# Optimization experiments

Measured on AMD Instinct MI355X. Metric: run time of the kernel, lower is better.

## Reference

```python
import jax, jax.numpy as jnp
import numpy as np

N_NODES = 100000
N_EDGES = 1600000
N_GRAPHS = 64


def setup_inputs() -> dict:
    key = jax.random.key(0)
    ks = jax.random.split(key, 10)
    x = jax.random.normal(ks[0], (N_NODES, 2), jnp.float32)
    edge_index = jax.random.randint(ks[1], (2, N_EDGES), 0, N_NODES, dtype=jnp.int64)
    batch_index = jnp.sort(jax.random.randint(ks[2], (N_NODES,), 0, N_GRAPHS, dtype=jnp.int64))

    def glorot(k, shape):
        return jax.random.normal(k, shape, jnp.float32) * jnp.sqrt(2.0 / (shape[0] + shape[1]))

    return {
        "x": x,
        "edge_index": edge_index,
        "batch_index": batch_index,
        "W1": glorot(ks[3], (2, 8)),   "b1": jnp.zeros((8,), jnp.float32),
        "W2": glorot(ks[4], (8, 32)),  "b2": jnp.zeros((32,), jnp.float32),
        "W3": glorot(ks[5], (32, 128)),"b3": jnp.zeros((128,), jnp.float32),
        "Wl": glorot(ks[6], (128, 3)), "bl": jnp.zeros((3,), jnp.float32),
    }


def _gcn_conv(x, W, b, src, dst, norm, n):
    # GCNConv: linear transform, then normalized scatter-add aggregation, then bias.
    h = x @ W                                     # [N, out]
    msg = h[src] * norm[:, None]                  # [E', out] gather + scale
    agg = jax.ops.segment_sum(msg, dst, num_segments=n)
    return agg + b


def reference(x, edge_index, batch_index, W1, b1, W2, b2, W3, b3, Wl, bl):
    n = x.shape[0]
    loop = jnp.arange(n, dtype=edge_index.dtype)
    src = jnp.concatenate([edge_index[0], loop])  # add self-loops (GCNConv default)
    dst = jnp.concatenate([edge_index[1], loop])
    # symmetric normalization D^{-1/2} (A+I) D^{-1/2}
    deg = jax.ops.segment_sum(jnp.ones_like(dst, dtype=x.dtype), dst, num_segments=n)
    dis = jnp.where(deg > 0, jax.lax.rsqrt(jnp.maximum(deg, 1.0)), 0.0)
    norm = dis[src] * dis[dst]

    h = jax.nn.relu(_gcn_conv(x, W1, b1, src, dst, norm, n))
    h = jax.nn.relu(_gcn_conv(h, W2, b2, src, dst, norm, n))  # dropout is identity in eval
    h = _gcn_conv(h, W3, b3, src, dst, norm, n)               # [N, 128]
    pooled = jax.ops.segment_max(h, batch_index, num_segments=N_GRAPHS)  # global_max_pool
    logits = pooled @ Wl + bl                                  # [G, 3]
    return jax.nn.log_softmax(logits, axis=1)
```

## Files before the change

### kernel.cpp

```cpp
#include <hip/hip_runtime.h>


#define BSHIFT 9
#define BSZ 512
#define P2_TILE 2048
#define P1_BLOCKS 128

__device__ __forceinline__ unsigned fenc(float x) {
  unsigned b = __float_as_uint(x);
  return (b & 0x80000000u) ? ~b : (b | 0x80000000u);
}
__device__ __forceinline__ float fdec(unsigned k) {
  return (k & 0x80000000u) ? __uint_as_float(k ^ 0x80000000u)
                           : __uint_as_float(~k);
}


__global__ __launch_bounds__(256) void p1_hist_kernel(const int* __restrict__ dst,
                                                      int* __restrict__ hist2d, int E) {
  __shared__ int h[256];
  h[threadIdx.x] = 0;
  __syncthreads();
  for (int e = blockIdx.x * blockDim.x + threadIdx.x; e < E; e += gridDim.x * blockDim.x)
    atomicAdd(&h[dst[e] >> BSHIFT], 1);
  __syncthreads();
  hist2d[blockIdx.x * 256 + threadIdx.x] = h[threadIdx.x];
}

__global__ __launch_bounds__(256) void p1_scan_kernel(const int* __restrict__ hist2d,
                                                      int* __restrict__ bucketBase,
                                                      int* __restrict__ bucketCursor,
                                                      unsigned* __restrict__ pooled,
                                                      int B, int E, int G) {
  __shared__ int s[256];
  int t = threadIdx.x;
  int v = 0;
  for (int b = 0; b < P1_BLOCKS; ++b) v += hist2d[b * 256 + t];
  if (t >= B) v = 0;
  s[t] = v;
  __syncthreads();
  for (int o = 1; o < 256; o <<= 1) {
    int u = (t >= o) ? s[t - o] : 0;
    __syncthreads();
    s[t] += u;
    __syncthreads();
  }
  int excl = s[t] - v;
  bucketBase[t] = excl;
  bucketCursor[t] = excl;
  if (t == 0) bucketBase[256] = E;
  for (int i = t; i < G * 128; i += 256) pooled[i] = 0u;
}

__global__ __launch_bounds__(256) void p2_partition_kernel(
    const int* __restrict__ src, const int* __restrict__ dst,
    int* __restrict__ bucketCursor, unsigned* __restrict__ part, int E) {
  __shared__ int hist[256];
  __shared__ int lbase[256];
  __shared__ int gbase[256];
  __shared__ int cur[256];
  __shared__ unsigned sbuf[P2_TILE];
  __shared__ unsigned abuf[P2_TILE];
  int t = threadIdx.x;
  int e0 = blockIdx.x * P2_TILE;
  int cnt = min(P2_TILE, E - e0);

  hist[t] = 0;
  __syncthreads();

  int myb[P2_TILE / 256];
  unsigned myp[P2_TILE / 256];
#pragma unroll
  for (int k = 0; k < P2_TILE / 256; ++k) {
    int i = t + k * 256;
    if (i < cnt) {
      int e = e0 + i;
      int d = dst[e];
      int b = d >> BSHIFT;
      myb[k] = b;
      myp[k] = ((unsigned)(d & (BSZ - 1)) << 17) | (unsigned)src[e];
      atomicAdd(&hist[b], 1);
    } else {
      myb[k] = -1;
      myp[k] = 0;
    }
  }
  __syncthreads();

  int v = hist[t];
  lbase[t] = v;
  __syncthreads();
  for (int o = 1; o < 256; o <<= 1) {
    int u = (t >= o) ? lbase[t - o] : 0;
    __syncthreads();
    lbase[t] += u;
    __syncthreads();
  }
  int excl = lbase[t] - v;
  __syncthreads();
  lbase[t] = excl;
  if (v > 0) gbase[t] = atomicAdd(&bucketCursor[t], v);
  cur[t] = 0;
  __syncthreads();

#pragma unroll
  for (int k = 0; k < P2_TILE / 256; ++k) {
    int b = myb[k];
    if (b >= 0) {
      int pos = atomicAdd(&cur[b], 1);
      int li = lbase[b] + pos;
      sbuf[li] = myp[k];
      abuf[li] = (unsigned)(gbase[b] + pos);
    }
  }
  __syncthreads();

#pragma unroll
  for (int k = 0; k < P2_TILE / 256; ++k) {
    int i = t + k * 256;
    if (i < cnt) part[abuf[i]] = sbuf[i];
  }
}

__global__ __launch_bounds__(512) void p3_build_kernel(
    const unsigned* __restrict__ part, const int* __restrict__ bucketBase,
    const float* __restrict__ x, float* __restrict__ xs,
    float* __restrict__ dis, int* __restrict__ rp, int* __restrict__ csr,
    int N, int B, int E) {
  __shared__ int hist[BSZ];
  __shared__ int scn[BSZ];
  int b = blockIdx.x, t = threadIdx.x;
  int base = bucketBase[b], end = bucketBase[b + 1];
  int cnt = end - base;

  hist[t] = 0;
  __syncthreads();
  for (int i = t; i < cnt; i += BSZ) atomicAdd(&hist[part[base + i] >> 17], 1);
  __syncthreads();

  int v = hist[t];
  scn[t] = v;
  __syncthreads();
  for (int o = 1; o < BSZ; o <<= 1) {
    int u = (t >= o) ? scn[t - o] : 0;
    __syncthreads();
    scn[t] += u;
    __syncthreads();
  }
  int excl = scn[t] - v;

  int n = (b << BSHIFT) + t;
  if (n < N) {
    float dn = rsqrtf((float)v + 1.0f);
    dis[n] = dn;
    rp[n] = base + excl;
    float2 xn = *reinterpret_cast<const float2*>(x + 2 * (size_t)n);
    float2 o;
    o.x = dn * xn.x;
    o.y = dn * xn.y;
    *reinterpret_cast<float2*>(xs + 2 * (size_t)n) = o;
  }
  if (b == B - 1 && t == 0) rp[N] = E;

  hist[t] = excl;
  __syncthreads();
  for (int i = t; i < cnt; i += BSZ) {
    unsigned p = part[base + i];
    int pos = atomicAdd(&hist[p >> 17], 1);
    csr[base + pos] = (int)(p & 0x1FFFFu);
  }
}


__global__ __launch_bounds__(256) void layer1_kernel(
    const int* __restrict__ rp, const int* __restrict__ csr, const float* __restrict__ dis,
    const float* __restrict__ xs, const float* __restrict__ W1, const float* __restrict__ b1,
    float* __restrict__ h1s, int N) {
  __shared__ float sW[16];
  __shared__ float sb[8];
  int t = threadIdx.x;
  if (t < 16) sW[t] = W1[t];
  if (t < 8) sb[t] = b1[t];
  __syncthreads();
  int n = blockIdx.x * blockDim.x + t;
  if (n >= N) return;
  float2 a = *reinterpret_cast<const float2*>(xs + 2 * (size_t)n);
  int j0 = rp[n], j1 = rp[n + 1];
#pragma unroll 4
  for (int j = j0; j < j1; ++j) {
    int s = csr[j];
    const float2 v = *reinterpret_cast<const float2*>(xs + 2 * (size_t)s);
    a.x += v.x;
    a.y += v.y;
  }
  float dn = dis[n];
  float ax = dn * a.x, ay = dn * a.y;
  float4 o0, o1;
  float* o = &o0.x;
#pragma unroll
  for (int f = 0; f < 8; ++f)
    o[f] = dn * fmaxf(ax * sW[f] + ay * sW[8 + f] + sb[f], 0.f);
  *reinterpret_cast<float4*>(h1s + (size_t)n * 8) = o0;
  *reinterpret_cast<float4*>(h1s + (size_t)n * 8 + 4) = o1;
}

__global__ __launch_bounds__(256) void layer2_kernel(
    const int* __restrict__ rp, const int* __restrict__ csr, const float* __restrict__ dis,
    const float* __restrict__ h1s, const float* __restrict__ W2, const float* __restrict__ b2,
    float* __restrict__ h2s, int N) {
  __shared__ float sW[256];
  __shared__ float sb[32];
  int t = threadIdx.x;
  sW[t] = W2[t];
  if (t < 32) sb[t] = b2[t];
  __syncthreads();
  int n = blockIdx.x * blockDim.x + t;
  if (n >= N) return;
  float4 a0 = *reinterpret_cast<const float4*>(h1s + (size_t)n * 8);
  float4 a1 = *reinterpret_cast<const float4*>(h1s + (size_t)n * 8 + 4);
  int j0 = rp[n], j1 = rp[n + 1];
#pragma unroll 2
  for (int j = j0; j < j1; ++j) {
    int s = csr[j];
    const float4 v0 = *reinterpret_cast<const float4*>(h1s + (size_t)s * 8);
    const float4 v1 = *reinterpret_cast<const float4*>(h1s + (size_t)s * 8 + 4);
    a0.x += v0.x; a0.y += v0.y; a0.z += v0.z; a0.w += v0.w;
    a1.x += v1.x; a1.y += v1.y; a1.z += v1.z; a1.w += v1.w;
  }
  float dn = dis[n];
  float a2r[8] = {dn * a0.x, dn * a0.y, dn * a0.z, dn * a0.w,
                  dn * a1.x, dn * a1.y, dn * a1.z, dn * a1.w};
#pragma unroll
  for (int fc = 0; fc < 8; ++fc) {
    float4 o;
    o.x = sb[fc * 4 + 0]; o.y = sb[fc * 4 + 1]; o.z = sb[fc * 4 + 2]; o.w = sb[fc * 4 + 3];
#pragma unroll
    for (int k = 0; k < 8; ++k) {
      const float4 w = *reinterpret_cast<const float4*>(&sW[k * 32 + fc * 4]);
      float a = a2r[k];
      o.x += a * w.x; o.y += a * w.y; o.z += a * w.z; o.w += a * w.w;
    }
    o.x = dn * fmaxf(o.x, 0.f);
    o.y = dn * fmaxf(o.y, 0.f);
    o.z = dn * fmaxf(o.z, 0.f);
    o.w = dn * fmaxf(o.w, 0.f);
    *reinterpret_cast<float4*>(h2s + (size_t)n * 32 + fc * 4) = o;
  }
}

__global__ __launch_bounds__(128) void layer3_pool_kernel(
    const int* __restrict__ rp, const int* __restrict__ csr, const float* __restrict__ dis,
    const float* __restrict__ h2s, const float* __restrict__ W3, const float* __restrict__ b3,
    const int* __restrict__ batch, unsigned* __restrict__ pooled, int N) {
  __shared__ float rows[16][32];
  int t = threadIdx.x;
  float Wreg[32];
#pragma unroll
  for (int k = 0; k < 32; ++k) Wreg[k] = W3[k * 128 + t];
  float bb = b3[t];

  int n0 = blockIdx.x * 16;
  int m = min(16, N - n0);

  {
    int r = t >> 3;
    int n = n0 + r;
    if (r < m) {
      int off = (t & 7) * 4;
      float4 acc = *reinterpret_cast<const float4*>(h2s + (size_t)n * 32 + off);
      int j0 = rp[n], j1 = rp[n + 1];
#pragma unroll 4
      for (int j = j0; j < j1; ++j) {
        int s = csr[j];
        const float4 v = *reinterpret_cast<const float4*>(h2s + (size_t)s * 32 + off);
        acc.x += v.x; acc.y += v.y; acc.z += v.z; acc.w += v.w;
      }
      float dn = dis[n];
      rows[r][off + 0] = dn * acc.x;
      rows[r][off + 1] = dn * acc.y;
      rows[r][off + 2] = dn * acc.z;
      rows[r][off + 3] = dn * acc.w;
    }
  }
  __syncthreads();

  int curg = batch[n0];
  float runmax = -INFINITY;
  for (int r = 0; r < m; ++r) {
    int g = batch[n0 + r];
    if (g != curg) {
      atomicMax(&pooled[(size_t)curg * 128 + t], fenc(runmax));
      runmax = -INFINITY;
      curg = g;
    }
    float acc = bb;
#pragma unroll
    for (int k = 0; k < 32; ++k) acc += rows[r][k] * Wreg[k];
    runmax = fmaxf(runmax, acc);
  }
  atomicMax(&pooled[(size_t)curg * 128 + t], fenc(runmax));
}

__global__ __launch_bounds__(128) void head_kernel(
    const unsigned* __restrict__ pooled, const float* __restrict__ Wl,
    const float* __restrict__ bl, float* __restrict__ out, int G) {
  int g = blockIdx.x;
  int t = threadIdx.x;
  float p = fdec(pooled[(size_t)g * 128 + t]);
  __shared__ float red[128];
  __shared__ float sj[3];
  for (int j = 0; j < 3; ++j) {
    red[t] = p * Wl[t * 3 + j];
    __syncthreads();
    for (int k = 64; k > 0; k >>= 1) {
      if (t < k) red[t] += red[t + k];
      __syncthreads();
    }
    if (t == 0) sj[j] = red[0];
    __syncthreads();
  }
  if (t == 0) {
    float l0 = sj[0] + bl[0], l1 = sj[1] + bl[1], l2 = sj[2] + bl[2];
    float m = fmaxf(l0, fmaxf(l1, l2));
    float lse = logf(expf(l0 - m) + expf(l1 - m) + expf(l2 - m));
    out[g * 3 + 0] = l0 - m - lse;
    out[g * 3 + 1] = l1 - m - lse;
    out[g * 3 + 2] = l2 - m - lse;
  }
}

extern "C" void kernel_launch(void* const* d_in, const int* in_sizes, int n_in,
                              void* d_out, int out_size, void* d_ws, size_t ws_size,
                              hipStream_t stream) {
  const float* x = (const float*)d_in[0];
  const int* ei = (const int*)d_in[1];
  const int* batch = (const int*)d_in[2];
  const float* W1 = (const float*)d_in[3];
  const float* b1 = (const float*)d_in[4];
  const float* W2 = (const float*)d_in[5];
  const float* b2 = (const float*)d_in[6];
  const float* W3 = (const float*)d_in[7];
  const float* b3 = (const float*)d_in[8];
  const float* Wl = (const float*)d_in[9];
  const float* bl = (const float*)d_in[10];
  float* out = (float*)d_out;

  const int N = in_sizes[0] / 2;
  const int E = in_sizes[1] / 2;
  const int G = out_size / 3;

  const int* src = ei;
  const int* dstp = ei + E;

  const int B = (N + BSZ - 1) / BSZ;

  size_t NP = ((size_t)N + 256) & ~(size_t)255;
  size_t EP = ((size_t)E + 255) & ~(size_t)255;

  float* dis = (float*)d_ws;
  int* rp = (int*)d_ws + NP;
  int* csr = rp + NP;
  unsigned* part = (unsigned*)(csr + EP);
  int* bucketBase = (int*)(part + EP);
  int* bucketCursor = bucketBase + 512;
  int* hist2d = bucketCursor + 512;
  float* arena = (float*)(hist2d + P1_BLOCKS * 256);

  float* xs = arena;
  float* h1s = arena + (size_t)2 * N;
  float* h2s = arena + (size_t)10 * N;
  unsigned* pooled = (unsigned*)(arena + (size_t)42 * N);

  const int BS = 256;
  auto cdiv = [](long long a, long long b) { return (int)((a + b - 1) / b); };

  p1_hist_kernel<<<P1_BLOCKS, 256, 0, stream>>>(dstp, hist2d, E);
  p1_scan_kernel<<<1, 256, 0, stream>>>(hist2d, bucketBase, bucketCursor, pooled, B, E, G);
  p2_partition_kernel<<<cdiv(E, P2_TILE), 256, 0, stream>>>(src, dstp, bucketCursor, part, E);
  p3_build_kernel<<<B, BSZ, 0, stream>>>(part, bucketBase, x, xs, dis, rp, csr, N, B, E);

  layer1_kernel<<<cdiv(N, BS), BS, 0, stream>>>(rp, csr, dis, xs, W1, b1, h1s, N);
  layer2_kernel<<<cdiv(N, BS), BS, 0, stream>>>(rp, csr, dis, h1s, W2, b2, h2s, N);
  layer3_pool_kernel<<<cdiv(N, 16), 128, 0, stream>>>(rp, csr, dis, h2s, W3, b3, batch, pooled, N);

  head_kernel<<<G, 128, 0, stream>>>(pooled, Wl, bl, out, G);
}
```

Measured before the change: 147.8 us.

## Balance layer-3 gather across block edges using packed local-row ids in CSR

After: 388.4 us. 2.63x slower.

```diff
diff --git a/kernel.cpp b/kernel.cpp
--- a/kernel.cpp
+++ b/kernel.cpp
@@ -5,6 +5,7 @@
 #define BSZ 512
 #define P2_TILE 2048
 #define P1_BLOCKS 128
+#define SRCMASK 0x1FFFF
 
 __device__ __forceinline__ unsigned fenc(float x) {
   unsigned b = __float_as_uint(x);
@@ -125,7 +126,7 @@
 __global__ __launch_bounds__(512) void p3_build_kernel(
     const unsigned* __restrict__ part, const int* __restrict__ bucketBase,
     const float* __restrict__ x, float* __restrict__ xs,
-    float* __restrict__ dis, int* __restrict__ rp, int* __restrict__ csr,
+    float* __restrict__ dis, int* __restrict__ rp, unsigned* __restrict__ csr,
     int N, int B, int E) {
   __shared__ int hist[BSZ];
   __shared__ int scn[BSZ];
@@ -166,14 +167,15 @@
   __syncthreads();
   for (int i = t; i < cnt; i += BSZ) {
     unsigned p = part[base + i];
-    int pos = atomicAdd(&hist[p >> 17], 1);
-    csr[base + pos] = (int)(p & 0x1FFFFu);
+    unsigned dl = p >> 17;
+    int pos = atomicAdd(&hist[dl], 1);
+    csr[base + pos] = (p & SRCMASK) | ((dl & 15u) << 28);
   }
 }
 
 
 __global__ __launch_bounds__(256) void layer1_kernel(
-    const int* __restrict__ rp, const int* __restrict__ csr, const float* __restrict__ dis,
+    const int* __restrict__ rp, const unsigned* __restrict__ csr, const float* __restrict__ dis,
     const float* __restrict__ xs, const float* __restrict__ W1, const float* __restrict__ b1,
     float* __restrict__ h1s, int N) {
   __shared__ float sW[16];
@@ -188,7 +190,7 @@
   int j0 = rp[n], j1 = rp[n + 1];
 #pragma unroll 4
   for (int j = j0; j < j1; ++j) {
-    int s = csr[j];
+    int s = csr[j] & SRCMASK;
     const float2 v = *reinterpret_cast<const float2*>(xs + 2 * (size_t)s);
     a.x += v.x;
     a.y += v.y;
@@ -205,7 +207,7 @@
 }
 
 __global__ __launch_bounds__(256) void layer2_kernel(
-    const int* __restrict__ rp, const int* __restrict__ csr, const float* __restrict__ dis,
+    const int* __restrict__ rp, const unsigned* __restrict__ csr, const float* __restrict__ dis,
     const float* __restrict__ h1s, const float* __restrict__ W2, const float* __restrict__ b2,
     float* __restrict__ h2s, int N) {
   __shared__ float sW[256];
@@ -221,7 +223,7 @@
   int j0 = rp[n], j1 = rp[n + 1];
 #pragma unroll 2
   for (int j = j0; j < j1; ++j) {
-    int s = csr[j];
+    int s = csr[j] & SRCMASK;
     const float4 v0 = *reinterpret_cast<const float4*>(h1s + (size_t)s * 8);
     const float4 v1 = *reinterpret_cast<const float4*>(h1s + (size_t)s * 8 + 4);
     a0.x += v0.x; a0.y += v0.y; a0.z += v0.z; a0.w += v0.w;
@@ -249,10 +251,11 @@
 }
 
 __global__ __launch_bounds__(128) void layer3_pool_kernel(
-    const int* __restrict__ rp, const int* __restrict__ csr, const float* __restrict__ dis,
+    const int* __restrict__ rp, const unsigned* __restrict__ csr, const float* __restrict__ dis,
     const float* __restrict__ h2s, const float* __restrict__ W3, const float* __restrict__ b3,
     const int* __restrict__ batch, unsigned* __restrict__ pooled, int N) {
   __shared__ float rows[16][32];
+  __shared__ float dnv[16];
   int t = threadIdx.x;
   float Wreg[32];
 #pragma unroll
@@ -261,42 +264,46 @@
 
   int n0 = blockIdx.x * 16;
   int m = min(16, N - n0);
-
-  {
-    int r = t >> 3;
-    int n = n0 + r;
-    if (r < m) {
-      int off = (t & 7) * 4;
-      float4 acc = *reinterpret_cast<const float4*>(h2s + (size_t)n * 32 + off);
-      int j0 = rp[n], j1 = rp[n + 1];
-#pragma unroll 4
-      for (int j = j0; j < j1; ++j) {
-        int s = csr[j];
-        const float4 v = *reinterpret_cast<const float4*>(h2s + (size_t)s * 32 + off);
-        acc.x += v.x; acc.y += v.y; acc.z += v.z; acc.w += v.w;
-      }
-      float dn = dis[n];
-      rows[r][off + 0] = dn * acc.x;
-      rows[r][off + 1] = dn * acc.y;
-      rows[r][off + 2] = dn * acc.z;
-      rows[r][off + 3] = dn * acc.w;
-    }
+  int r = t >> 3;
+  int off = (t & 7) * 4;
+
+  if (r < m) {
+    const float4 sv = *reinterpret_cast<const float4*>(h2s + (size_t)(n0 + r) * 32 + off);
+    rows[r][off + 0] = sv.x;
+    rows[r][off + 1] = sv.y;
+    rows[r][off + 2] = sv.z;
+    rows[r][off + 3] = sv.w;
+  }
+  if (t < m) dnv[t] = dis[n0 + t];
+  __syncthreads();
+
+  int j0 = rp[n0];
+  int cnt = rp[n0 + m] - j0;
+  for (int idx = r; idx < cnt; idx += 16) {
+    unsigned p = csr[j0 + idx];
+    int s = p & SRCMASK;
+    int lr = p >> 28;
+    const float4 v = *reinterpret_cast<const float4*>(h2s + (size_t)s * 32 + off);
+    atomicAdd(&rows[lr][off + 0], v.x);
+    atomicAdd(&rows[lr][off + 1], v.y);
+    atomicAdd(&rows[lr][off + 2], v.z);
+    atomicAdd(&rows[lr][off + 3], v.w);
   }
   __syncthreads();
 
   int curg = batch[n0];
   float runmax = -INFINITY;
-  for (int r = 0; r < m; ++r) {
-    int g = batch[n0 + r];
+  for (int q = 0; q < m; ++q) {
+    int g = batch[n0 + q];
     if (g != curg) {
       atomicMax(&pooled[(size_t)curg * 128 + t], fenc(runmax));
       runmax = -INFINITY;
       curg = g;
     }
-    float acc = bb;
-#pragma unroll
-    for (int k = 0; k < 32; ++k) acc += rows[r][k] * Wreg[k];
-    runmax = fmaxf(runmax, acc);
+    float acc = 0.f;
+#pragma unroll
+    for (int k = 0; k < 32; ++k) acc += rows[q][k] * Wreg[k];
+    runmax = fmaxf(runmax, dnv[q] * acc + bb);
   }
   atomicMax(&pooled[(size_t)curg * 128 + t], fenc(runmax));
 }
@@ -359,7 +366,7 @@
 
   float* dis = (float*)d_ws;
   int* rp = (int*)d_ws + NP;
-  int* csr = rp + NP;
+  unsigned* csr = (unsigned*)(rp + NP);
   unsigned* part = (unsigned*)(csr + EP);
   int* bucketBase = (int*)(part + EP);
   int* bucketCursor = bucketBase + 512;
```

## Store layer-2 activations in fp16 and widen layer-3 gather per block

Applied to the files above, without the earlier changes.

New measurement: 138.8 us. -6.1%, faster.

```diff
diff --git a/kernel.cpp b/kernel.cpp
--- a/kernel.cpp
+++ b/kernel.cpp
@@ -1,10 +1,13 @@
 #include <hip/hip_runtime.h>
+#include <hip/hip_fp16.h>
 
 
 #define BSHIFT 9
 #define BSZ 512
 #define P2_TILE 2048
 #define P1_BLOCKS 128
+#define SRCMASK 0x1FFFF
+#define NB3 32
 
 __device__ __forceinline__ unsigned fenc(float x) {
   unsigned b = __float_as_uint(x);
@@ -13,6 +16,14 @@
 __device__ __forceinline__ float fdec(unsigned k) {
   return (k & 0x80000000u) ? __uint_as_float(k ^ 0x80000000u)
                            : __uint_as_float(~k);
+}
+__device__ __forceinline__ unsigned pack2(float a, float b) {
+  __half2 h = __floats2half2_rn(a, b);
+  return *reinterpret_cast<unsigned*>(&h);
+}
+__device__ __forceinline__ float2 unpack2(unsigned u) {
+  __half2 h = *reinterpret_cast<__half2*>(&u);
+  return __half22float2(h);
 }
 
 
@@ -125,7 +136,7 @@
 __global__ __launch_bounds__(512) void p3_build_kernel(
     const unsigned* __restrict__ part, const int* __restrict__ bucketBase,
     const float* __restrict__ x, float* __restrict__ xs,
-    float* __restrict__ dis, int* __restrict__ rp, int* __restrict__ csr,
+    float* __restrict__ dis, int* __restrict__ rp, unsigned* __restrict__ csr,
     int N, int B, int E) {
   __shared__ int hist[BSZ];
   __shared__ int scn[BSZ];
@@ -167,13 +178,13 @@
   for (int i = t; i < cnt; i += BSZ) {
     unsigned p = part[base + i];
     int pos = atomicAdd(&hist[p >> 17], 1);
-    csr[base + pos] = (int)(p & 0x1FFFFu);
+    csr[base + pos] = p & SRCMASK;
   }
 }
 
 
 __global__ __launch_bounds__(256) void layer1_kernel(
-    const int* __restrict__ rp, const int* __restrict__ csr, const float* __restrict__ dis,
+    const int* __restrict__ rp, const unsigned* __restrict__ csr, const float* __restrict__ dis,
     const float* __restrict__ xs, const float* __restrict__ W1, const float* __restrict__ b1,
     float* __restrict__ h1s, int N) {
   __shared__ float sW[16];
@@ -205,9 +216,9 @@
 }
 
 __global__ __launch_bounds__(256) void layer2_kernel(
-    const int* __restrict__ rp, const int* __restrict__ csr, const float* __restrict__ dis,
+    const int* __restrict__ rp, const unsigned* __restrict__ csr, const float* __restrict__ dis,
     const float* __restrict__ h1s, const float* __restrict__ W2, const float* __restrict__ b2,
-    float* __restrict__ h2s, int N) {
+    __half* __restrict__ h2h, int N) {
   __shared__ float sW[256];
   __shared__ float sb[32];
   int t = threadIdx.x;
@@ -219,7 +230,7 @@
   float4 a0 = *reinterpret_cast<const float4*>(h1s + (size_t)n * 8);
   float4 a1 = *reinterpret_cast<const float4*>(h1s + (size_t)n * 8 + 4);
   int j0 = rp[n], j1 = rp[n + 1];
-#pragma unroll 2
+#pragma unroll 4
   for (int j = j0; j < j1; ++j) {
     int s = csr[j];
     const float4 v0 = *reinterpret_cast<const float4*>(h1s + (size_t)s * 8);
@@ -230,6 +241,8 @@
   float dn = dis[n];
   float a2r[8] = {dn * a0.x, dn * a0.y, dn * a0.z, dn * a0.w,
                   dn * a1.x, dn * a1.y, dn * a1.z, dn * a1.w};
+  uint4 pk[4];
+  unsigned* pw = &pk[0].x;
 #pragma unroll
   for (int fc = 0; fc < 8; ++fc) {
     float4 o;
@@ -244,45 +257,54 @@
     o.y = dn * fmaxf(o.y, 0.f);
     o.z = dn * fmaxf(o.z, 0.f);
     o.w = dn * fmaxf(o.w, 0.f);
-    *reinterpret_cast<float4*>(h2s + (size_t)n * 32 + fc * 4) = o;
-  }
+    pw[fc * 2 + 0] = pack2(o.x, o.y);
+    pw[fc * 2 + 1] = pack2(o.z, o.w);
+  }
+  uint4* dst16 = reinterpret_cast<uint4*>(h2h + (size_t)n * 32);
+  dst16[0] = pk[0];
+  dst16[1] = pk[1];
+  dst16[2] = pk[2];
+  dst16[3] = pk[3];
 }
 
 __global__ __launch_bounds__(128) void layer3_pool_kernel(
-    const int* __restrict__ rp, const int* __restrict__ csr, const float* __restrict__ dis,
-    const float* __restrict__ h2s, const float* __restrict__ W3, const float* __restrict__ b3,
+    const int* __restrict__ rp, const unsigned* __restrict__ csr, const float* __restrict__ dis,
+    const __half* __restrict__ h2h, const float* __restrict__ W3, const float* __restrict__ b3,
     const int* __restrict__ batch, unsigned* __restrict__ pooled, int N) {
-  __shared__ float rows[16][32];
-  int t = threadIdx.x;
+  __shared__ float rows[NB3][32];
+  __shared__ float dnv[NB3];
+  int t = threadIdx.x;
+  int gi = t >> 2;
+  int q = t & 3;
+
+  int n0 = blockIdx.x * NB3;
+  int m = min(NB3, N - n0);
+
+  if (t < m) dnv[t] = dis[n0 + t];
+
+  if (gi < m) {
+    int n = n0 + gi;
+    uint4 sv = *reinterpret_cast<const uint4*>(h2h + (size_t)n * 32 + q * 8);
+    float2 f0 = unpack2(sv.x), f1 = unpack2(sv.y), f2 = unpack2(sv.z), f3 = unpack2(sv.w);
+    float acc[8] = {f0.x, f0.y, f1.x, f1.y, f2.x, f2.y, f3.x, f3.y};
+    int j0 = rp[n], j1 = rp[n + 1];
+#pragma unroll 4
+    for (int j = j0; j < j1; ++j) {
+      int s = csr[j];
+      uint4 v = *reinterpret_cast<const uint4*>(h2h + (size_t)s * 32 + q * 8);
+      float2 g0 = unpack2(v.x), g1 = unpack2(v.y), g2 = unpack2(v.z), g3 = unpack2(v.w);
+      acc[0] += g0.x; acc[1] += g0.y; acc[2] += g1.x; acc[3] += g1.y;
+      acc[4] += g2.x; acc[5] += g2.y; acc[6] += g3.x; acc[7] += g3.y;
+    }
+#pragma unroll
+    for (int i = 0; i < 8; ++i) rows[gi][q * 8 + i] = acc[i];
+  }
+  __syncthreads();
+
   float Wreg[32];
 #pragma unroll
   for (int k = 0; k < 32; ++k) Wreg[k] = W3[k * 128 + t];
   float bb = b3[t];
-
-  int n0 = blockIdx.x * 16;
-  int m = min(16, N - n0);
-
-  {
-    int r = t >> 3;
-    int n = n0 + r;
-    if (r < m) {
-      int off = (t & 7) * 4;
-      float4 acc = *reinterpret_cast<const float4*>(h2s + (size_t)n * 32 + off);
-      int j0 = rp[n], j1 = rp[n + 1];
-#pragma unroll 4
-      for (int j = j0; j < j1; ++j) {
-        int s = csr[j];
-        const float4 v = *reinterpret_cast<const float4*>(h2s + (size_t)s * 32 + off);
-        acc.x += v.x; acc.y += v.y; acc.z += v.z; acc.w += v.w;
-      }
-      float dn = dis[n];
-      rows[r][off + 0] = dn * acc.x;
-      rows[r][off + 1] = dn * acc.y;
-      rows[r][off + 2] = dn * acc.z;
-      rows[r][off + 3] = dn * acc.w;
-    }
-  }
-  __syncthreads();
 
   int curg = batch[n0];
   float runmax = -INFINITY;
@@ -293,10 +315,10 @@
       runmax = -INFINITY;
       curg = g;
     }
-    float acc = bb;
+    float acc = 0.f;
 #pragma unroll
     for (int k = 0; k < 32; ++k) acc += rows[r][k] * Wreg[k];
-    runmax = fmaxf(runmax, acc);
+    runmax = fmaxf(runmax, dnv[r] * acc + bb);
   }
   atomicMax(&pooled[(size_t)curg * 128 + t], fenc(runmax));
 }
@@ -359,7 +381,7 @@
 
   float* dis = (float*)d_ws;
   int* rp = (int*)d_ws + NP;
-  int* csr = rp + NP;
+  unsigned* csr = (unsigned*)(rp + NP);
   unsigned* part = (unsigned*)(csr + EP);
   int* bucketBase = (int*)(part + EP);
   int* bucketCursor = bucketBase + 512;
@@ -368,8 +390,8 @@
 
   float* xs = arena;
   float* h1s = arena + (size_t)2 * N;
-  float* h2s = arena + (size_t)10 * N;
-  unsigned* pooled = (unsigned*)(arena + (size_t)42 * N);
+  __half* h2h = (__half*)(arena + (size_t)10 * N);
+  unsigned* pooled = (unsigned*)(arena + (size_t)26 * N);
 
   const int BS = 256;
   auto cdiv = [](long long a, long long b) { return (int)((a + b - 1) / b); };
@@ -380,8 +402,8 @@
   p3_build_kernel<<<B, BSZ, 0, stream>>>(part, bucketBase, x, xs, dis, rp, csr, N, B, E);
 
   layer1_kernel<<<cdiv(N, BS), BS, 0, stream>>>(rp, csr, dis, xs, W1, b1, h1s, N);
-  layer2_kernel<<<cdiv(N, BS), BS, 0, stream>>>(rp, csr, dis, h1s, W2, b2, h2s, N);
-  layer3_pool_kernel<<<cdiv(N, 16), 128, 0, stream>>>(rp, csr, dis, h2s, W3, b3, batch, pooled, N);
+  layer2_kernel<<<cdiv(N, BS), BS, 0, stream>>>(rp, csr, dis, h1s, W2, b2, h2h, N);
+  layer3_pool_kernel<<<cdiv(N, NB3), 128, 0, stream>>>(rp, csr, dis, h2h, W3, b3, batch, pooled, N);
 
   head_kernel<<<G, 128, 0, stream>>>(pooled, Wl, bl, out, G);
 }
```
